# Optimization experiments

Measured on AMD Instinct MI355X. Metric: run time of the kernel, lower is better.

Reference implementation:

```python
import jax, jax.numpy as jnp
import numpy as np

D = 128          # hidden_channels
NU = 50000       # num user nodes
NI = 50000       # num item nodes
E = 600000       # edges per edge type
SLOPE = 0.01     # F.leaky_relu default negative_slope


def setup_inputs() -> dict:
    key = jax.random.key(0)
    ks = jax.random.split(key, 24)
    ws = 1.0 / np.sqrt(D)  # xavier-ish scale

    def W2(i):  # stacked [n_layers=2, D, D] weight
        return jax.random.normal(ks[i], (2, D, D), jnp.float32) * ws

    def B2(i):  # stacked [2, D] bias
        return jax.random.normal(ks[i], (2, D), jnp.float32) * 0.01

    inp = {
        "x_user": jax.random.normal(ks[0], (NU, D), jnp.float32),
        "x_item": jax.random.normal(ks[1], (NI, D), jnp.float32),
        # row 0 = src indices, row 1 = dst indices
        "ei_ui": jax.random.randint(ks[2], (2, E), 0, NU),  # user -> item (dst in [0,NI))
        "ei_iu": jax.random.randint(ks[3], (2, E), 0, NI),  # item -> user (dst in [0,NU))
        # per-node-type q/k/v Linear params, stacked over the 2 layers
        "q_w_user": W2(4),  "q_b_user": B2(5),
        "k_w_user": W2(6),  "k_b_user": B2(7),
        "v_w_user": W2(8),  "v_b_user": B2(9),
        "q_w_item": W2(10), "q_b_item": B2(11),
        "k_w_item": W2(12), "k_b_item": B2(13),
        "v_w_item": W2(14), "v_b_item": B2(15),
        # per-edge-type bilinear W, stacked over the 2 layers
        "W_ui": W2(16),
        "W_iu": W2(17),
    }
    return inp


def _edge_agg(x_src, x_dst, qw, qb, kw, kb, vw, vb, W, src, dst, n_dst):
    # torch Linear: x @ w.T + b
    q = x_src @ qw.T + qb            # [Nsrc, D]
    k = x_dst @ kw.T + kb            # [Ndst, D]
    v = x_src @ vw.T + vb            # [Nsrc, D]
    qW = q @ W                       # project on nodes (cheaper than per-edge)
    # per-edge bilinear score q_src . W . k_dst / sqrt(D)
    score = jnp.sum(qW[src] * k[dst], axis=-1) * (1.0 / np.sqrt(D))  # [E]
    alpha = jax.nn.softmax(jax.nn.leaky_relu(score, SLOPE))          # softmax over edges
    msg = alpha[:, None] * v[src]                                    # [E, D]
    return jax.ops.segment_sum(msg, dst, num_segments=n_dst)


def _layer(x_u, x_i, ei_ui, ei_iu, p, l):
    # edge type (user, rates, item): q/v from src type (user), k from dst type (item)
    agg_i = _edge_agg(x_u, x_i,
                      p["q_w_user"][l], p["q_b_user"][l],
                      p["k_w_item"][l], p["k_b_item"][l],
                      p["v_w_user"][l], p["v_b_user"][l],
                      p["W_ui"][l], ei_ui[0], ei_ui[1], NI)
    # edge type (item, rev_rates, user)
    agg_u = _edge_agg(x_i, x_u,
                      p["q_w_item"][l], p["q_b_item"][l],
                      p["k_w_user"][l], p["k_b_user"][l],
                      p["v_w_item"][l], p["v_b_item"][l],
                      p["W_iu"][l], ei_iu[0], ei_iu[1], NU)
    # out_dict initialized with x_dst.clone(), then scatter_add
    return x_u + agg_u, x_i + agg_i


def reference(x_user, x_item, ei_ui, ei_iu,
              q_w_user, q_b_user, k_w_user, k_b_user, v_w_user, v_b_user,
              q_w_item, q_b_item, k_w_item, k_b_item, v_w_item, v_b_item,
              W_ui, W_iu):
    p = dict(q_w_user=q_w_user, q_b_user=q_b_user, k_w_user=k_w_user,
             k_b_user=k_b_user, v_w_user=v_w_user, v_b_user=v_b_user,
             q_w_item=q_w_item, q_b_item=q_b_item, k_w_item=k_w_item,
             k_b_item=k_b_item, v_w_item=v_w_item, v_b_item=v_b_item,
             W_ui=W_ui, W_iu=W_iu)
    x_u, x_i = _layer(x_user, x_item, ei_ui, ei_iu, p, 0)  # conv1
    x_u, x_i = _layer(x_u, x_i, ei_ui, ei_iu, p, 1)        # conv2
    return jnp.concatenate([x_u, x_i], axis=0)  # [NU+NI, D]
```

## Files before the change

kernel.cpp:

```cpp
#include <hip/hip_runtime.h>
#include <stdint.h>

#define D 128

typedef __attribute__((ext_vector_type(8))) short bf16x8;
typedef __attribute__((ext_vector_type(4))) float f32x4;
typedef __attribute__((ext_vector_type(2))) float f32x2;
typedef unsigned short u16;
typedef unsigned char u8;
typedef unsigned int u32;

#define KSCALE (0.08838834764831845f * 1.4426950408889634f)

#if defined(__has_builtin)
#if __has_builtin(__builtin_amdgcn_cvt_pk_f32_fp8) && __has_builtin(__builtin_amdgcn_cvt_pk_fp8_f32)
#define HW_FP8 1
#endif
#if __has_builtin(__builtin_elementwise_fma)
#define VFMA(a, b, c) __builtin_elementwise_fma(a, b, c)
#else
#define VFMA(a, b, c) ((a) * (b) + (c))
#endif
#else
#define VFMA(a, b, c) ((a) * (b) + (c))
#endif

static __device__ __forceinline__ float b2f(u16 u) {
  return __uint_as_float(((unsigned)u) << 16);
}
static __device__ __forceinline__ u16 f2b(float f) {
  unsigned u = __float_as_uint(f);
  return (u16)((u + 0x7fffu + ((u >> 16) & 1u)) >> 16);
}

static __device__ __forceinline__ u8 enc_fp8(float f) {
#ifdef HW_FP8
  int p = __builtin_amdgcn_cvt_pk_fp8_f32(f, 0.f, 0, false);
  return (u8)(p & 0xff);
#else
  float a = fabsf(f);
  unsigned s = (__float_as_uint(f) >> 31) << 7;
  if (a < 7.8125e-3f) {
    int m = (int)(a * 512.f + 0.5f);
    if (m > 7) m = 7;
    return (u8)(s | m);
  }
  int e; float mant = frexpf(a, &e);
  int E = e + 6;
  int m = (int)((2.f * mant - 1.f) * 8.f + 0.5f);
  if (m == 8) { m = 0; E++; }
  if (E > 15 || (E == 15 && m > 6)) { E = 15; m = 6; }
  if (E < 1) return (u8)s;
  return (u8)(s | (E << 3) | m);
#endif
}

static __device__ __forceinline__ float dec1_fp8(u8 b) {
  int e = (b >> 3) & 15, m = b & 7;
  float mag = e ? ldexpf((float)(8 + m), e - 10) : ldexpf((float)m, -9);
  return (b & 128) ? -mag : mag;
}

static __device__ __forceinline__ void dec8_fp8_v(u32 lo, u32 hi, f32x2* o) {
#ifdef HW_FP8
  o[0] = __builtin_amdgcn_cvt_pk_f32_fp8((int)lo, false);
  o[1] = __builtin_amdgcn_cvt_pk_f32_fp8((int)lo, true);
  o[2] = __builtin_amdgcn_cvt_pk_f32_fp8((int)hi, false);
  o[3] = __builtin_amdgcn_cvt_pk_f32_fp8((int)hi, true);
#else
  u32 w[2] = {lo, hi};
  u8* p = (u8*)w;
#pragma unroll
  for (int i = 0; i < 4; ++i) o[i] = (f32x2){dec1_fp8(p[2 * i]), dec1_fp8(p[2 * i + 1])};
#endif
}

template <int CTRL>
static __device__ __forceinline__ float dpp_add_f(float x) {
  int y = __builtin_amdgcn_update_dpp(0, __float_as_int(x), CTRL, 0xf, 0xf, true);
  return x + __int_as_float(y);
}

__global__ void prep_fused(const float* __restrict__ qwu, const float* __restrict__ qbu,
                           const float* __restrict__ qwi, const float* __restrict__ qbi,
                           const float* __restrict__ Wui, const float* __restrict__ Wiu,
                           u16* __restrict__ Mt, float* __restrict__ bq) {
  int c = blockIdx.y, d = blockIdx.x, j = threadIdx.x;
  int l = c & 1, type = c >> 1;
  const float* qw = (type ? qwi : qwu) + l * D * D;
  const float* qb = (type ? qbi : qbu) + l * D;
  const float* W  = (type ? Wiu : Wui) + l * D * D;
  float acc = 0.f;
  for (int cc = 0; cc < D; ++cc) acc += qw[cc * D + d] * W[cc * D + j];
  Mt[((size_t)c * D + j) * D + d] = f2b(acc);
  if (d == 0) {
    float ba = 0.f;
    for (int cc = 0; cc < D; ++cc) ba += qb[cc] * W[cc * D + j];
    bq[c * D + j] = ba;
  }
}

__global__ void cast_w(const float* __restrict__ kwu, const float* __restrict__ kwi,
                       const float* __restrict__ vwu, const float* __restrict__ vwi,
                       u16* __restrict__ Wb) {
  int y = blockIdx.y;
  const float* s = (y == 0) ? kwu : (y == 1) ? kwi : (y == 2) ? vwu : vwi;
  int i = blockIdx.x * 256 + threadIdx.x;
  Wb[(size_t)y * 2 * D * D + i] = f2b(s[i]);
}

__global__ void cast_x(const float* __restrict__ x, u16* __restrict__ xb, int n2) {
  int i = blockIdx.x * 256 + threadIdx.x;
  if (i < n2) {
    float2 v = ((const float2*)x)[i];
    ((unsigned*)xb)[i] = (unsigned)f2b(v.x) | ((unsigned)f2b(v.y) << 16);
  }
}

__global__ void zero_i(int* __restrict__ p, int n) {
  int i = blockIdx.x * 256 + threadIdx.x;
  if (i < n) p[i] = 0;
}

__global__ __launch_bounds__(256) void bhist(const int* __restrict__ dui,
                                             const int* __restrict__ diu,
                                             int* __restrict__ cnt_ui,
                                             int* __restrict__ cnt_iu, int E) {
  __shared__ int h[256];
  int t = threadIdx.x;
  h[t] = 0;
  __syncthreads();
  const int* dp = blockIdx.y ? diu : dui;
  int e0 = blockIdx.x * 1024;
#pragma unroll
  for (int i = 0; i < 4; ++i) {
    int e = e0 + i * 256 + t;
    if (e < E) atomicAdd(&h[dp[e] >> 8], 1);
  }
  __syncthreads();
  int* out = blockIdx.y ? cnt_iu : cnt_ui;
  if (h[t]) atomicAdd(&out[t], h[t]);
}

__global__ __launch_bounds__(256) void bscan(const int* __restrict__ cnt_ui,
                                             const int* __restrict__ cnt_iu,
                                             int* __restrict__ base_ui, int* __restrict__ base_iu,
                                             int* __restrict__ cur_ui, int* __restrict__ cur_iu,
                                             int* __restrict__ rp_ui, int* __restrict__ rp_iu,
                                             int nb_ui, int nb_iu, int n_ui, int n_iu, int E) {
  __shared__ int sh[256];
  int t = threadIdx.x;
  int v = (t < nb_ui) ? cnt_ui[t] : 0;
  sh[t] = v;
  __syncthreads();
  for (int off = 1; off < 256; off <<= 1) {
    int u = (t >= off) ? sh[t - off] : 0;
    __syncthreads();
    sh[t] += u;
    __syncthreads();
  }
  int ex = sh[t] - v;
  if (t < nb_ui) { base_ui[t] = ex; cur_ui[t] = ex; }
  if (t == 0) { base_ui[nb_ui] = E; rp_ui[n_ui] = E; }
  __syncthreads();
  v = (t < nb_iu) ? cnt_iu[t] : 0;
  sh[t] = v;
  __syncthreads();
  for (int off = 1; off < 256; off <<= 1) {
    int u = (t >= off) ? sh[t - off] : 0;
    __syncthreads();
    sh[t] += u;
    __syncthreads();
  }
  ex = sh[t] - v;
  if (t < nb_iu) { base_iu[t] = ex; cur_iu[t] = ex; }
  if (t == 0) { base_iu[nb_iu] = E; rp_iu[n_iu] = E; }
}

__global__ __launch_bounds__(256) void bscatter(
    const int* __restrict__ sui, const int* __restrict__ dui,
    const int* __restrict__ siu, const int* __restrict__ diu,
    int* __restrict__ cur_ui, int* __restrict__ cur_iu,
    u32* __restrict__ bb_ui, u32* __restrict__ bb_iu, int E) {
  __shared__ int h[256], rbase[256], c2[256];
  int t = threadIdx.x;
  const int* sp = blockIdx.y ? siu : sui;
  const int* dp = blockIdx.y ? diu : dui;
  int* gc = blockIdx.y ? cur_iu : cur_ui;
  u32* bb = blockIdx.y ? bb_iu : bb_ui;
  h[t] = 0;
  c2[t] = 0;
  __syncthreads();
  int e0 = blockIdx.x * 1024;
  u32 pr[4];
  int bk[4];
  bool act[4];
#pragma unroll
  for (int i = 0; i < 4; ++i) {
    int e = e0 + i * 256 + t;
    act[i] = e < E;
    if (act[i]) {
      int s = sp[e], d2 = dp[e];
      pr[i] = ((u32)d2 << 16) | (u32)s;
      bk[i] = d2 >> 8;
      atomicAdd(&h[bk[i]], 1);
    }
  }
  __syncthreads();
  if (h[t]) rbase[t] = atomicAdd(&gc[t], h[t]);
  __syncthreads();
#pragma unroll
  for (int i = 0; i < 4; ++i) {
    if (act[i]) {
      int r = atomicAdd(&c2[bk[i]], 1);
      bb[rbase[bk[i]] + r] = pr[i];
    }
  }
}

__global__ __launch_bounds__(256) void bsort(
    const u32* __restrict__ bb_ui, const u32* __restrict__ bb_iu,
    const int* __restrict__ base_ui, const int* __restrict__ base_iu,
    int* __restrict__ rp_ui, int* __restrict__ rp_iu,
    int* __restrict__ cs_ui, int* __restrict__ cs_iu,
    int nb_ui, int n_ui, int n_iu) {
  int b = blockIdx.x;
  const u32* bb; const int* base; int* rp; int* cs; int n;
  if (b < nb_ui) { bb = bb_ui; base = base_ui; rp = rp_ui; cs = cs_ui; n = n_ui; }
  else { b -= nb_ui; bb = bb_iu; base = base_iu; rp = rp_iu; cs = cs_iu; n = n_iu; }
  int lo = base[b], hi = base[b + 1];
  __shared__ int h[256], sh[256], cur[256];
  int t = threadIdx.x;
  h[t] = 0;
  __syncthreads();
  for (int j = lo + t; j < hi; j += 256) atomicAdd(&h[(bb[j] >> 16) & 255], 1);
  __syncthreads();
  int v = h[t];
  sh[t] = v;
  __syncthreads();
  for (int off = 1; off < 256; off <<= 1) {
    int u = (t >= off) ? sh[t - off] : 0;
    __syncthreads();
    sh[t] += u;
    __syncthreads();
  }
  int ex = lo + sh[t] - v;
  int gd = (b << 8) + t;
  if (gd < n) rp[gd] = ex;
  cur[t] = ex;
  __syncthreads();
  for (int j = lo + t; j < hi; j += 256) {
    u32 pr = bb[j];
    int p = atomicAdd(&cur[(pr >> 16) & 255], 1);
    cs[p] = (int)(pr & 0xffffu);
  }
}

__global__ __launch_bounds__(256) void gemm3(
    const u16* __restrict__ xu, const u16* __restrict__ xi,
    const u16* __restrict__ wqu, const u16* __restrict__ wku, const u16* __restrict__ wvu,
    const float* __restrict__ bqu, const float* __restrict__ bku, const float* __restrict__ bvu,
    const u16* __restrict__ wqi, const u16* __restrict__ wki, const u16* __restrict__ wvi,
    const float* __restrict__ bqi, const float* __restrict__ bki, const float* __restrict__ bvi,
    u8* __restrict__ Tqv_u, u16* __restrict__ Tk_u,
    u8* __restrict__ Tqv_i, u16* __restrict__ Tk_i,
    int gu, int nu, int ni) {
  __shared__ __align__(16) u16 wlds[128 * 136];
  int bx = blockIdx.x, y = blockIdx.y;
  bool item = bx >= gu;
  if (item) bx -= gu;
  const u16* x = item ? xi : xu;
  int nrows = item ? ni : nu;
  const u16* wt; const float* bias;
  if (y == 0)      { wt = item ? wqi : wqu; bias = item ? bqi : bqu; }
  else if (y == 1) { wt = item ? wki : wku; bias = item ? bki : bku; }
  else             { wt = item ? wvi : wvu; bias = item ? bvi : bvu; }
  u8* Tqv = item ? Tqv_i : Tqv_u;
  u16* Tk = item ? Tk_i : Tk_u;

  int t = threadIdx.x;
#pragma unroll
  for (int i = 0; i < 8; ++i) {
    int idx = t + 256 * i;
    int n = idx >> 4, kc = idx & 15;
    ((bf16x8*)wlds)[n * 17 + kc] = ((const bf16x8*)wt)[idx];
  }
  __syncthreads();
  int wave = t >> 6, lane = t & 63;
  int m = lane & 15, quad = lane >> 4;
  int row0 = bx * 64 + wave * 16;
  int arow = row0 + m;
  const bf16x8* xv = (const bf16x8*)(x + (size_t)(arow < nrows ? arow : 0) * D);
  f32x4 acc[8];
#pragma unroll
  for (int n = 0; n < 8; ++n) acc[n] = (f32x4){0.f, 0.f, 0.f, 0.f};
#pragma unroll
  for (int kk = 0; kk < 4; ++kk) {
    bf16x8 a = xv[kk * 4 + quad];
#pragma unroll
    for (int n = 0; n < 8; ++n) {
      bf16x8 b = ((const bf16x8*)wlds)[(n * 16 + m) * 17 + kk * 4 + quad];
      acc[n] = __builtin_amdgcn_mfma_f32_16x16x32_bf16(a, b, acc[n], 0, 0, 0);
    }
  }
  __syncthreads();
  if (y == 1) {
    u16* ob = (u16*)wlds;
#pragma unroll
    for (int n = 0; n < 8; ++n) {
      float bb = bias[n * 16 + m];
#pragma unroll
      for (int r = 0; r < 4; ++r) {
        int rl = wave * 16 + quad * 4 + r;
        ob[rl * 136 + n * 16 + m] = f2b((acc[n][r] + bb) * KSCALE);
      }
    }
    __syncthreads();
    int rl = t >> 2, c0 = (t & 3) * 32;
    int orow = bx * 64 + rl;
    if (orow < nrows) {
      const uint4* src = (const uint4*)(ob + rl * 136 + c0);
      uint4* dst = (uint4*)(Tk + (size_t)orow * 128 + c0);
      dst[0] = src[0]; dst[1] = src[1]; dst[2] = src[2]; dst[3] = src[3];
    }
  } else {
    int vo = (y == 0) ? 0 : 128;
    u8* ob = (u8*)wlds;
#pragma unroll
    for (int n = 0; n < 8; ++n) {
      float bb = bias[n * 16 + m];
#pragma unroll
      for (int r = 0; r < 4; ++r) {
        int rl = wave * 16 + quad * 4 + r;
        ob[rl * 144 + n * 16 + m] = enc_fp8(acc[n][r] + bb);
      }
    }
    __syncthreads();
    int rl = t >> 2, c0 = (t & 3) * 32;
    int orow = bx * 64 + rl;
    if (orow < nrows) {
      const uint4* src = (const uint4*)(ob + rl * 144 + c0);
      uint4* dst = (uint4*)(Tqv + (size_t)orow * 256 + vo + c0);
      dst[0] = src[0]; dst[1] = src[1];
    }
  }
}

static __device__ __forceinline__ void do_edge(uint2 qw, uint2 vw, bool act,
                                               const f32x2* kx, f32x2* acc, float& z) {
  f32x2 qx[4], vx[4];
  dec8_fp8_v(qw.x, qw.y, qx);
  dec8_fp8_v(vw.x, vw.y, vx);
  f32x2 d2 = qx[0] * kx[0];
  d2 = VFMA(qx[1], kx[1], d2);
  d2 = VFMA(qx[2], kx[2], d2);
  d2 = VFMA(qx[3], kx[3], d2);
  float dot = d2.x + d2.y;
  dot = dpp_add_f<0xB1>(dot);
  dot = dpp_add_f<0x4E>(dot);
  dot = dpp_add_f<0x128>(dot);
  dot = dpp_add_f<0x124>(dot);
  float sc = (dot > 0.f) ? dot : 0.01f * dot;
  float p = act ? exp2f(sc) : 0.f;
  z += p;
  f32x2 p2 = {p, p};
  acc[0] = VFMA(p2, vx[0], acc[0]);
  acc[1] = VFMA(p2, vx[1], acc[1]);
  acc[2] = VFMA(p2, vx[2], acc[2]);
  acc[3] = VFMA(p2, vx[3], acc[3]);
}

__global__ __launch_bounds__(256, 8) void agg_pass(
    const u8* __restrict__ Tqv_u, const u16* __restrict__ Tk_u,
    const u8* __restrict__ Tqv_i, const u16* __restrict__ Tk_i,
    const int* __restrict__ rp_ui, const int* __restrict__ cs_ui,
    const int* __restrict__ rp_iu, const int* __restrict__ cs_iu,
    float* __restrict__ agg_u, float* __restrict__ agg_i,
    float* __restrict__ zpart, int gai, int ni, int nu) {
  int bx = blockIdx.x;
  const u8* Pqv; const u16* Pk; const int* rp; const int* cs;
  float* agg; float* zp; int ndst;
  if (bx < gai) { Pqv = Tqv_u; Pk = Tk_i; rp = rp_ui; cs = cs_ui; agg = agg_i; zp = zpart; ndst = ni; }
  else { bx -= gai; Pqv = Tqv_i; Pk = Tk_u; rp = rp_iu; cs = cs_iu; agg = agg_u; zp = zpart + 1024; ndst = nu; }
  int wave = threadIdx.x >> 6, lane = threadIdx.x & 63;
  int d = bx * 4 + wave;
  int sub = lane & 15;
  int quad = lane >> 4;
  float z = 0.f;
  f32x2 acc[4] = {{0.f, 0.f}, {0.f, 0.f}, {0.f, 0.f}, {0.f, 0.f}};
  if (d < ndst) {
    bf16x8 kf = *(const bf16x8*)(Pk + (size_t)d * D + sub * 8);
    int beg = rp[d], end = rp[d + 1];
    f32x2 kx[4];
#pragma unroll
    for (int i = 0; i < 4; ++i)
      kx[i] = (f32x2){b2f((u16)((short*)&kf)[2 * i]), b2f((u16)((short*)&kf)[2 * i + 1])};
    const u8* Pq = Pqv + sub * 8;
    for (int j = beg; j < end; j += 16) {
      int rem = end - j;
      int e1 = end - 1;
      int i0 = j + quad, i1 = i0 + 4, i2 = i0 + 8, i3 = i0 + 12;
      int s0 = cs[i0 < end ? i0 : e1];
      int s1 = cs[i1 < end ? i1 : e1];
      int s2 = cs[i2 < end ? i2 : e1];
      int s3 = cs[i3 < end ? i3 : e1];
      const u8* b0 = Pq + (size_t)s0 * 256;
      const u8* b1 = Pq + (size_t)s1 * 256;
      const u8* b2 = Pq + (size_t)s2 * 256;
      const u8* b3 = Pq + (size_t)s3 * 256;
      uint2 q0 = *(const uint2*)b0;
      uint2 q1 = *(const uint2*)b1;
      uint2 q2 = *(const uint2*)b2;
      uint2 q3 = *(const uint2*)b3;
      uint2 v0 = *(const uint2*)(b0 + 128);
      uint2 v1 = *(const uint2*)(b1 + 128);
      uint2 v2 = *(const uint2*)(b2 + 128);
      uint2 v3 = *(const uint2*)(b3 + 128);
      do_edge(q0, v0, i0 < end, kx, acc, z);
      if (rem > 4)  do_edge(q1, v1, i1 < end, kx, acc, z);
      if (rem > 8)  do_edge(q2, v2, i2 < end, kx, acc, z);
      if (rem > 12) do_edge(q3, v3, i3 < end, kx, acc, z);
    }
    float* af = (float*)acc;
#pragma unroll
    for (int i = 0; i < 8; ++i) {
      af[i] += __shfl_xor(af[i], 16, 64);
      af[i] += __shfl_xor(af[i], 32, 64);
    }
    if (quad == 0) {
      float* ap = agg + (size_t)d * D + sub * 8;
      __builtin_nontemporal_store((f32x4){af[0], af[1], af[2], af[3]}, (f32x4*)ap);
      __builtin_nontemporal_store((f32x4){af[4], af[5], af[6], af[7]}, (f32x4*)ap + 1);
    }
    z += __shfl_xor(z, 16, 64);
    z += __shfl_xor(z, 32, 64);
  }
  __shared__ float ps[4];
  if (lane == 0) ps[wave] = z;
  __syncthreads();
  if (threadIdx.x == 0)
    unsafeAtomicAdd(&zp[blockIdx.x & 1023], ps[0] + ps[1] + ps[2] + ps[3]);
}

__global__ void update_x(const float* __restrict__ xu, const float* __restrict__ xi,
                         const float* __restrict__ aggu, const float* __restrict__ aggi,
                         const float* __restrict__ zpart,
                         float* __restrict__ ou, float* __restrict__ oi,
                         u16* __restrict__ bu, u16* __restrict__ bi,
                         int nu4, int ni4, int wb) {
  __shared__ float red0[256], red1[256];
  int t = threadIdx.x;
  float s0 = zpart[t] + zpart[t + 256] + zpart[t + 512] + zpart[t + 768];
  float s1 = zpart[1024 + t] + zpart[1280 + t] + zpart[1536 + t] + zpart[1792 + t];
  red0[t] = s0;
  red1[t] = s1;
  __syncthreads();
  for (int k = 128; k > 0; k >>= 1) {
    if (t < k) { red0[t] += red0[t + k]; red1[t] += red1[t + k]; }
    __syncthreads();
  }
  float zi = 1.0f / red0[0];
  float zu = 1.0f / red1[0];
  int i = blockIdx.x * 256 + t;
  const float4* xs; const float4* as; float4* os; u16* bs; float zz; int jj;
  if (i < nu4) {
    xs = (const float4*)xu; as = (const float4*)aggu; os = (float4*)ou; bs = bu;
    zz = zu; jj = i;
  } else if (i < nu4 + ni4) {
    jj = i - nu4;
    xs = (const float4*)xi; as = (const float4*)aggi; os = (float4*)oi; bs = bi;
    zz = zi;
  } else {
    return;
  }
  float4 xv = xs[jj];
  float4 av = as[jj];
  float4 v;
  v.x = xv.x + av.x * zz;
  v.y = xv.y + av.y * zz;
  v.z = xv.z + av.z * zz;
  v.w = xv.w + av.w * zz;
  os[jj] = v;
  if (wb) {
    ushort4 b;
    b.x = f2b(v.x); b.y = f2b(v.y); b.z = f2b(v.z); b.w = f2b(v.w);
    ((ushort4*)bs)[jj] = b;
  }
}

extern "C" void kernel_launch(void* const* d_in, const int* in_sizes, int n_in,
                              void* d_out, int out_size, void* d_ws, size_t ws_size,
                              hipStream_t stream) {
  const float* xu_in = (const float*)d_in[0];
  const float* xi_in = (const float*)d_in[1];
  const int* ei_ui = (const int*)d_in[2];
  const int* ei_iu = (const int*)d_in[3];
  const float* qwu = (const float*)d_in[4];
  const float* qbu = (const float*)d_in[5];
  const float* kwu = (const float*)d_in[6];
  const float* kbu = (const float*)d_in[7];
  const float* vwu = (const float*)d_in[8];
  const float* vbu = (const float*)d_in[9];
  const float* qwi = (const float*)d_in[10];
  const float* qbi = (const float*)d_in[11];
  const float* kwi = (const float*)d_in[12];
  const float* kbi = (const float*)d_in[13];
  const float* vwi = (const float*)d_in[14];
  const float* vbi = (const float*)d_in[15];
  const float* Wui = (const float*)d_in[16];
  const float* Wiu = (const float*)d_in[17];

  int NU = in_sizes[0] / D;
  int NI = in_sizes[1] / D;
  int E  = in_sizes[2] / 2;

  char* w = (char*)d_ws;
  float* agg_u = (float*)w;  w += (size_t)NU * D * 4;
  float* agg_i = (float*)w;  w += (size_t)NI * D * 4;
  int* bcnt_ui = (int*)w;    w += 256 * 4;
  int* bcnt_iu = (int*)w;    w += 256 * 4;
  float* zpart = (float*)w;  w += 4096 * 4;
  float* bq    = (float*)w;  w += 4 * D * 4;
  int* base_ui = (int*)w;    w += 260 * 4;
  int* base_iu = (int*)w;    w += 260 * 4;
  int* cur_ui  = (int*)w;    w += 256 * 4;
  int* cur_iu  = (int*)w;    w += 256 * 4;
  int* rp_ui = (int*)w;      w += (size_t)(NI + 4) * 4;
  int* rp_iu = (int*)w;      w += (size_t)(NU + 4) * 4;
  int* cs_ui = (int*)w;      w += (size_t)E * 4;
  int* cs_iu = (int*)w;      w += (size_t)E * 4;
  u32* bb_ui = (u32*)w;      w += (size_t)E * 4;
  u32* bb_iu = (u32*)w;      w += (size_t)E * 4;
  u16* Mt  = (u16*)w;        w += (size_t)4 * D * D * 2;
  u16* Wb  = (u16*)w;        w += (size_t)8 * D * D * 2;
  u16* xub = (u16*)w;        w += (size_t)NU * D * 2;
  u16* xib = (u16*)w;        w += (size_t)NI * D * 2;
  w = (char*)(((uintptr_t)w + 255) & ~(uintptr_t)255);
  u16* Tk_u = (u16*)w;       w += (size_t)NU * D * 2;
  u16* Tk_i = (u16*)w;       w += (size_t)NI * D * 2;
  u8* Tqv_u = (u8*)w;        w += (size_t)NU * 256;
  u8* Tqv_i = (u8*)w;

  float* out_u = (float*)d_out;
  float* out_i = out_u + (size_t)NU * D;

  prep_fused<<<dim3(128, 4), 128, 0, stream>>>(qwu, qbu, qwi, qbi, Wui, Wiu, Mt, bq);
  cast_w<<<dim3(128, 4), 256, 0, stream>>>(kwu, kwi, vwu, vwi, Wb);
  cast_x<<<(NU * D / 2 + 255) / 256, 256, 0, stream>>>(xu_in, xub, NU * D / 2);
  cast_x<<<(NI * D / 2 + 255) / 256, 256, 0, stream>>>(xi_in, xib, NI * D / 2);

  int nb_ui = (NI + 255) >> 8;
  int nb_iu = (NU + 255) >> 8;
  zero_i<<<18, 256, 0, stream>>>(bcnt_ui, 512 + 4096);
  int geb = (E + 1023) / 1024;
  bhist<<<dim3(geb, 2), 256, 0, stream>>>(ei_ui + E, ei_iu + E, bcnt_ui, bcnt_iu, E);
  bscan<<<1, 256, 0, stream>>>(bcnt_ui, bcnt_iu, base_ui, base_iu, cur_ui, cur_iu,
                               rp_ui, rp_iu, nb_ui, nb_iu, NI, NU, E);
  bscatter<<<dim3(geb, 2), 256, 0, stream>>>(ei_ui, ei_ui + E, ei_iu, ei_iu + E,
                                             cur_ui, cur_iu, bb_ui, bb_iu, E);
  bsort<<<nb_ui + nb_iu, 256, 0, stream>>>(bb_ui, bb_iu, base_ui, base_iu,
                                           rp_ui, rp_iu, cs_ui, cs_iu, nb_ui, NI, NU);

  int gu = (NU + 63) / 64, gi = (NI + 63) / 64;
  int gau = (NU + 3) / 4, gai = (NI + 3) / 4;
  int nu4 = NU * D / 4, ni4 = NI * D / 4;
  int gup = (nu4 + ni4 + 255) / 256;

  for (int l = 0; l < 2; ++l) {
    gemm3<<<dim3(gu + gi, 3), 256, 0, stream>>>(
        xub, xib,
        Mt + (size_t)l * D * D, Wb + (size_t)(0 + l) * D * D, Wb + (size_t)(4 + l) * D * D,
        bq + l * D, kbu + l * D, vbu + l * D,
        Mt + (size_t)(2 + l) * D * D, Wb + (size_t)(2 + l) * D * D, Wb + (size_t)(6 + l) * D * D,
        bq + (2 + l) * D, kbi + l * D, vbi + l * D,
        Tqv_u, Tk_u, Tqv_i, Tk_i, gu, NU, NI);
    agg_pass<<<gai + gau, 256, 0, stream>>>(
        Tqv_u, Tk_u, Tqv_i, Tk_i, rp_ui, cs_ui, rp_iu, cs_iu,
        agg_u, agg_i, zpart + (size_t)l * 2 * 1024, gai, NI, NU);
    if (l == 0)
      update_x<<<gup, 256, 0, stream>>>(xu_in, xi_in, agg_u, agg_i,
                                        zpart + (size_t)l * 2 * 1024,
                                        out_u, out_i, xub, xib, nu4, ni4, 1);
    else
      update_x<<<gup, 256, 0, stream>>>(out_u, out_i, agg_u, agg_i,
                                        zpart + (size_t)l * 2 * 1024,
                                        out_u, out_i, nullptr, nullptr, nu4, ni4, 0);
  }
}
```

Baseline: 450.9 us.

## Fuse q/k/v projections into one block per row tile reusing loaded activations

The gemm3 kernel previously launched three blocks per 64-row tile (one each for q, k, v), and each re-read the same activation rows. Now a single block loads the activation fragments into registers once and runs all three projections in turn, reloading each weight matrix into shared memory. The q results are kept packed in registers and written together with v as one 256-byte fp8 row. This cuts activation reads and grid size, but serialises the weight loads within a block, adds barriers, and raises register and LDS use, which may lower occupancy.

```diff
diff --git a/kernel.cpp b/kernel.cpp
--- a/kernel.cpp
+++ b/kernel.cpp
@@ -266,82 +266,131 @@
     u8* __restrict__ Tqv_i, u16* __restrict__ Tk_i,
     int gu, int nu, int ni) {
   __shared__ __align__(16) u16 wlds[128 * 136];
-  int bx = blockIdx.x, y = blockIdx.y;
+  __shared__ __align__(16) u16 outb[64 * 144];
+  int bx = blockIdx.x;
   bool item = bx >= gu;
   if (item) bx -= gu;
   const u16* x = item ? xi : xu;
   int nrows = item ? ni : nu;
-  const u16* wt; const float* bias;
-  if (y == 0)      { wt = item ? wqi : wqu; bias = item ? bqi : bqu; }
-  else if (y == 1) { wt = item ? wki : wku; bias = item ? bki : bku; }
-  else             { wt = item ? wvi : wvu; bias = item ? bvi : bvu; }
+  const u16* wq = item ? wqi : wqu;
+  const u16* wk = item ? wki : wku;
+  const u16* wv = item ? wvi : wvu;
+  const float* bq_ = item ? bqi : bqu;
+  const float* bk_ = item ? bki : bku;
+  const float* bv_ = item ? bvi : bvu;
   u8* Tqv = item ? Tqv_i : Tqv_u;
   u16* Tk = item ? Tk_i : Tk_u;
 
   int t = threadIdx.x;
-#pragma unroll
-  for (int i = 0; i < 8; ++i) {
-    int idx = t + 256 * i;
-    int n = idx >> 4, kc = idx & 15;
-    ((bf16x8*)wlds)[n * 17 + kc] = ((const bf16x8*)wt)[idx];
-  }
-  __syncthreads();
   int wave = t >> 6, lane = t & 63;
   int m = lane & 15, quad = lane >> 4;
   int row0 = bx * 64 + wave * 16;
   int arow = row0 + m;
   const bf16x8* xv = (const bf16x8*)(x + (size_t)(arow < nrows ? arow : 0) * D);
+  bf16x8 xa[4];
+#pragma unroll
+  for (int kk = 0; kk < 4; ++kk) xa[kk] = xv[kk * 4 + quad];
+
   f32x4 acc[8];
+  u32 qb[8];
+
+#pragma unroll
+  for (int i = 0; i < 8; ++i) {
+    int idx = t + 256 * i;
+    ((bf16x8*)wlds)[(idx >> 4) * 17 + (idx & 15)] = ((const bf16x8*)wq)[idx];
+  }
+  __syncthreads();
 #pragma unroll
   for (int n = 0; n < 8; ++n) acc[n] = (f32x4){0.f, 0.f, 0.f, 0.f};
 #pragma unroll
-  for (int kk = 0; kk < 4; ++kk) {
-    bf16x8 a = xv[kk * 4 + quad];
-#pragma unroll
-    for (int n = 0; n < 8; ++n) {
-      bf16x8 b = ((const bf16x8*)wlds)[(n * 16 + m) * 17 + kk * 4 + quad];
-      acc[n] = __builtin_amdgcn_mfma_f32_16x16x32_bf16(a, b, acc[n], 0, 0, 0);
-    }
-  }
-  __syncthreads();
-  if (y == 1) {
-    u16* ob = (u16*)wlds;
-#pragma unroll
-    for (int n = 0; n < 8; ++n) {
-      float bb = bias[n * 16 + m];
-#pragma unroll
-      for (int r = 0; r < 4; ++r) {
-        int rl = wave * 16 + quad * 4 + r;
-        ob[rl * 136 + n * 16 + m] = f2b((acc[n][r] + bb) * KSCALE);
-      }
-    }
-    __syncthreads();
+  for (int kk = 0; kk < 4; ++kk)
+#pragma unroll
+    for (int n = 0; n < 8; ++n)
+      acc[n] = __builtin_amdgcn_mfma_f32_16x16x32_bf16(
+          xa[kk], ((const bf16x8*)wlds)[(n * 16 + m) * 17 + kk * 4 + quad], acc[n], 0, 0, 0);
+#pragma unroll
+  for (int n = 0; n < 8; ++n) {
+    float bb = bq_[n * 16 + m];
+    u32 w4 = 0;
+#pragma unroll
+    for (int r = 0; r < 4; ++r) w4 |= (u32)enc_fp8(acc[n][r] + bb) << (8 * r);
+    qb[n] = w4;
+  }
+  __syncthreads();
+
+#pragma unroll
+  for (int i = 0; i < 8; ++i) {
+    int idx = t + 256 * i;
+    ((bf16x8*)wlds)[(idx >> 4) * 17 + (idx & 15)] = ((const bf16x8*)wk)[idx];
+  }
+  __syncthreads();
+#pragma unroll
+  for (int n = 0; n < 8; ++n) acc[n] = (f32x4){0.f, 0.f, 0.f, 0.f};
+#pragma unroll
+  for (int kk = 0; kk < 4; ++kk)
+#pragma unroll
+    for (int n = 0; n < 8; ++n)
+      acc[n] = __builtin_amdgcn_mfma_f32_16x16x32_bf16(
+          xa[kk], ((const bf16x8*)wlds)[(n * 16 + m) * 17 + kk * 4 + quad], acc[n], 0, 0, 0);
+#pragma unroll
+  for (int n = 0; n < 8; ++n) {
+    float bb = bk_[n * 16 + m];
+#pragma unroll
+    for (int r = 0; r < 4; ++r) {
+      int rl = wave * 16 + quad * 4 + r;
+      outb[rl * 136 + n * 16 + m] = f2b((acc[n][r] + bb) * KSCALE);
+    }
+  }
+  __syncthreads();
+
+  {
     int rl = t >> 2, c0 = (t & 3) * 32;
     int orow = bx * 64 + rl;
     if (orow < nrows) {
-      const uint4* src = (const uint4*)(ob + rl * 136 + c0);
+      const uint4* src = (const uint4*)(outb + rl * 136 + c0);
       uint4* dst = (uint4*)(Tk + (size_t)orow * 128 + c0);
       dst[0] = src[0]; dst[1] = src[1]; dst[2] = src[2]; dst[3] = src[3];
     }
-  } else {
-    int vo = (y == 0) ? 0 : 128;
-    u8* ob = (u8*)wlds;
+  }
+#pragma unroll
+  for (int i = 0; i < 8; ++i) {
+    int idx = t + 256 * i;
+    ((bf16x8*)wlds)[(idx >> 4) * 17 + (idx & 15)] = ((const bf16x8*)wv)[idx];
+  }
+  __syncthreads();
+
+#pragma unroll
+  for (int n = 0; n < 8; ++n) acc[n] = (f32x4){0.f, 0.f, 0.f, 0.f};
+#pragma unroll
+  for (int kk = 0; kk < 4; ++kk)
+#pragma unroll
+    for (int n = 0; n < 8; ++n)
+      acc[n] = __builtin_amdgcn_mfma_f32_16x16x32_bf16(
+          xa[kk], ((const bf16x8*)wlds)[(n * 16 + m) * 17 + kk * 4 + quad], acc[n], 0, 0, 0);
+  {
+    u8* ob8 = (u8*)outb;
 #pragma unroll
     for (int n = 0; n < 8; ++n) {
-      float bb = bias[n * 16 + m];
+      int dim = n * 16 + m;
+      float bb = bv_[dim];
 #pragma unroll
       for (int r = 0; r < 4; ++r) {
         int rl = wave * 16 + quad * 4 + r;
-        ob[rl * 144 + n * 16 + m] = enc_fp8(acc[n][r] + bb);
+        ob8[rl * 288 + dim] = (u8)(qb[n] >> (8 * r));
+        ob8[rl * 288 + 128 + dim] = enc_fp8(acc[n][r] + bb);
       }
     }
-    __syncthreads();
-    int rl = t >> 2, c0 = (t & 3) * 32;
+  }
+  __syncthreads();
+
+  {
+    const u8* ob8 = (const u8*)outb;
+    int rl = t >> 2, c0 = (t & 3) * 64;
     int orow = bx * 64 + rl;
     if (orow < nrows) {
-      const uint4* src = (const uint4*)(ob + rl * 144 + c0);
-      uint4* dst = (uint4*)(Tqv + (size_t)orow * 256 + vo + c0);
-      dst[0] = src[0]; dst[1] = src[1];
+      const uint4* src = (const uint4*)(ob8 + rl * 288 + c0);
+      uint4* dst = (uint4*)(Tqv + (size_t)orow * 256 + c0);
+      dst[0] = src[0]; dst[1] = src[1]; dst[2] = src[2]; dst[3] = src[3];
     }
   }
 }
@@ -567,7 +616,7 @@
   int gup = (nu4 + ni4 + 255) / 256;
 
   for (int l = 0; l < 2; ++l) {
-    gemm3<<<dim3(gu + gi, 3), 256, 0, stream>>>(
+    gemm3<<<gu + gi, 256, 0, stream>>>(
         xub, xib,
         Mt + (size_t)l * D * D, Wb + (size_t)(0 + l) * D * D, Wb + (size_t)(4 + l) * D * D,
         bq + l * D, kbu + l * D, vbu + l * D,
```

After: 457.5 us. No clear change (+1.5%).
